# Optimization experiments

Hardware: AMD Instinct MI355X
Metric: run time of the kernel (lower is better)

Reference implementation:

```python
import jax, jax.numpy as jnp
import numpy as np

N_TYPES = 4
N_RELS = 8
N, E, IN_DIM, OUT_DIM = 100000, 1600000, 64, 64
SQRT_DK = float(np.sqrt(OUT_DIM))  # num_heads = 1 -> d_k = out_dim


def setup_inputs() -> dict:
    key = jax.random.key(0)
    ks = jax.random.split(key, 12)
    s = 0.05  # keep activations well-scaled (xavier-ish)
    h = jax.random.normal(ks[0], (N, IN_DIM), jnp.float32)
    node_type = jax.random.randint(ks[1], (N,), 0, N_TYPES, jnp.int32)
    src = jax.random.randint(ks[2], (E,), 0, N, jnp.int32)
    dst = jax.random.randint(ks[3], (E,), 0, N, jnp.int32)
    etype = jax.random.randint(ks[4], (E,), 0, N_RELS, jnp.int32)
    k_lin = jax.random.normal(ks[5], (N_TYPES, IN_DIM, OUT_DIM), jnp.float32) * s
    q_lin = jax.random.normal(ks[6], (N_TYPES, IN_DIM, OUT_DIM), jnp.float32) * s
    v_lin = jax.random.normal(ks[7], (N_TYPES, IN_DIM, OUT_DIM), jnp.float32) * s
    a_lin = jax.random.normal(ks[8], (N_TYPES, OUT_DIM, OUT_DIM), jnp.float32) * s
    rel_att = jax.random.normal(ks[9], (N_RELS, OUT_DIM, OUT_DIM), jnp.float32) * s
    rel_msg = jax.random.normal(ks[10], (N_RELS, OUT_DIM, OUT_DIM), jnp.float32) * s
    rel_pri = jnp.ones((N_RELS,), jnp.float32)
    skip = jnp.ones((N_TYPES,), jnp.float32)
    return dict(h=h, node_type=node_type, src=src, dst=dst, etype=etype,
                k_lin=k_lin, q_lin=q_lin, v_lin=v_lin, a_lin=a_lin,
                rel_att=rel_att, rel_msg=rel_msg, rel_pri=rel_pri, skip=skip)


def _typed_matmul(x, W, node_type):
    # rgnn_relational_matmul_no_scatter_gather_list: per-node-type GEMM.
    # Small fixed loop over node types (4), masked accumulate.
    out = jnp.zeros((x.shape[0], W.shape[-1]), x.dtype)
    for t in range(W.shape[0]):
        out = out + jnp.where((node_type == t)[:, None], x @ W[t], 0.0)
    return out


def reference(h, node_type, src, dst, etype, k_lin, q_lin, v_lin, a_lin,
              rel_att, rel_msg, rel_pri, skip):
    # per-node-type K/Q/V projections (num_heads==1, d_k==out_dim)
    k = _typed_matmul(h, k_lin, node_type)  # [N, d_k]
    q = _typed_matmul(h, q_lin, node_type)  # [N, d_k]
    v = _typed_matmul(h, v_lin, node_type)  # [N, d_k]

    # q @ relation_att, computed per relation for ALL nodes then gathered per edge
    # (avoids materializing [E, d_k, d_k] relation weights per edge)
    qW = jnp.einsum('nd,rde->rne', q, rel_att)  # [R, N, d_k]
    t_edge = qW[etype, dst]                      # [E, d_k]  (dst-side product)
    # attention score: <q_dst @ W_att_r, k_src>
    score = jnp.sum(t_edge * k[src], axis=-1)    # [E]

    # edge softmax over incoming edges of each dst, scaled by pri/sqrt(d_k)
    logits = score * (rel_pri / SQRT_DK)[etype]
    m = jax.ops.segment_max(logits, dst, num_segments=N)
    ex = jnp.exp(logits - m[dst])
    den = jax.ops.segment_sum(ex, dst, num_segments=N)
    alpha = ex / jnp.where(den[dst] == 0, 1.0, den[dst])  # [E]

    # message: v_src @ W_msg_r, per relation then gathered per edge
    vW = jnp.einsum('nd,rde->rne', v, rel_msg)   # [R, N, d_k]
    msg = vW[etype, src]                          # [E, d_k]

    # softmax-weighted aggregation to dst nodes
    agg = jax.ops.segment_sum(alpha[:, None] * msg, dst, num_segments=N)  # [N, d_k]

    # output per-node-type GEMM with sigmoid(skip)-scaled a_linears
    W_out = jax.nn.sigmoid(skip)[:, None, None] * a_lin
    return _typed_matmul(agg, W_out, node_type)  # [N, out_dim]
```

## Files before the change

### kernel.cpp

```cpp
#include <hip/hip_runtime.h>
#include <math.h>

#define DIM 64
#define NT 4
#define NR 8

typedef __attribute__((ext_vector_type(8))) short bf16x8;
typedef __attribute__((ext_vector_type(8))) unsigned short u16x8;
typedef __attribute__((ext_vector_type(4))) float f32x4;

__device__ __forceinline__ unsigned short f2bf(float f) {
    unsigned u = __float_as_uint(f);
    return (unsigned short)((u + 0x7FFF + ((u >> 16) & 1)) >> 16);
}
__device__ __forceinline__ float bf2f(unsigned short u) {
    return __uint_as_float((unsigned)u << 16);
}
__device__ __forceinline__ bf16x8 ldb16(const unsigned short* p) {
    return *((const bf16x8*)p);
}

__global__ void type_count(const int* __restrict__ ntype, int* __restrict__ tm, int N) {
    int i = blockIdx.x * blockDim.x + threadIdx.x;
    int t = (i < N) ? ntype[i] : -1;
    int lane = threadIdx.x & 63;
    #pragma unroll
    for (int tt = 0; tt < NT; tt++) {
        unsigned long long m = __ballot(t == tt);
        int c = __popcll(m);
        if (c && lane == (__ffsll((long long)m) - 1)) atomicAdd(&tm[tt], c);
    }
}

__global__ void type_scan(int* __restrict__ tm) {
    if (threadIdx.x == 0 && blockIdx.x == 0) {
        int b = 0;
        for (int t = 0; t < NT; t++) { tm[4 + t] = b; b += ((tm[t] + 63) >> 6) << 6; }
        tm[12] = b;
    }
}

__global__ void type_scatter(const int* __restrict__ ntype, int* __restrict__ tm,
                             int* __restrict__ order, int N) {
    int i = blockIdx.x * blockDim.x + threadIdx.x;
    int t = (i < N) ? ntype[i] : -1;
    int lane = threadIdx.x & 63;
    #pragma unroll
    for (int tt = 0; tt < NT; tt++) {
        unsigned long long m = __ballot(t == tt);
        int c = __popcll(m);
        if (!c) continue;
        int ldr = __ffsll((long long)m) - 1;
        int base = 0;
        if (lane == ldr) base = atomicAdd(&tm[8 + tt], c);
        base = __shfl(base, ldr, 64);
        if (t == tt) {
            int rank = __popcll(m & ((1ull << lane) - 1ull));
            order[tm[4 + tt] + base + rank] = i;
        }
    }
}

__global__ void prep_all(const float* __restrict__ A, const float* __restrict__ Mw,
                         const float* __restrict__ kl, const float* __restrict__ ql,
                         const float* __restrict__ vl,
                         unsigned short* __restrict__ At, unsigned short* __restrict__ Mt,
                         unsigned short* __restrict__ Wkt, unsigned short* __restrict__ Wqt,
                         unsigned short* __restrict__ Wvt) {
    int i = blockIdx.x * blockDim.x + threadIdx.x;
    if (i >= 28 * DIM * DIM) return;
    int mat = i >> 12;
    int idx = i & 4095;
    int n = idx >> 6;
    int k = idx & 63;
    int so = k * DIM + n;
    if (mat < 8)       At [((size_t)mat << 12) + idx]        = f2bf(A [((size_t)mat << 12) + so]);
    else if (mat < 16) Mt [((size_t)(mat - 8) << 12) + idx]  = f2bf(Mw[((size_t)(mat - 8) << 12) + so]);
    else if (mat < 20) Wkt[((size_t)(mat - 16) << 12) + idx] = f2bf(kl[((size_t)(mat - 16) << 12) + so]);
    else if (mat < 24) Wqt[((size_t)(mat - 20) << 12) + idx] = f2bf(ql[((size_t)(mat - 20) << 12) + so]);
    else               Wvt[((size_t)(mat - 24) << 12) + idx] = f2bf(vl[((size_t)(mat - 24) << 12) + so]);
}

__global__ void __launch_bounds__(256)
proj_mfma(const float* __restrict__ h, const int* __restrict__ ntype,
          const int* __restrict__ order, const int* __restrict__ tm,
          const unsigned short* __restrict__ Wkt, const unsigned short* __restrict__ Wqt,
          const unsigned short* __restrict__ Wvt,
          unsigned short* __restrict__ kvbf, unsigned short* __restrict__ qbf, int N) {
    __shared__ __align__(16) unsigned short xs[64][72];
    int t  = threadIdx.x;
    int n0 = blockIdx.x * 64;
    if (n0 >= tm[12]) return;
    int first = order[n0];
    if (first < 0) return;
    int ty = ntype[first];

    #pragma unroll
    for (int i = 0; i < 4; i++) {
        int idx = t + 256 * i;
        int row = idx >> 4, c4 = idx & 15;
        int gn = order[n0 + row];
        float4 xv = make_float4(0.f, 0.f, 0.f, 0.f);
        if (gn >= 0) xv = ((const float4*)(h + (size_t)gn * DIM))[c4];
        ushort4 b = make_ushort4(f2bf(xv.x), f2bf(xv.y), f2bf(xv.z), f2bf(xv.w));
        *((ushort4*)&xs[row][c4 * 4]) = b;
    }
    __syncthreads();

    int wave = t >> 6, lane = t & 63;
    int m = lane & 15, quad = lane >> 4;
    bf16x8 xa0 = *((const bf16x8*)&xs[wave * 16 + m][quad * 8]);
    bf16x8 xa1 = *((const bf16x8*)&xs[wave * 16 + m][32 + quad * 8]);

    int g[4];
    #pragma unroll
    for (int reg = 0; reg < 4; reg++) g[reg] = order[n0 + wave * 16 + quad * 4 + reg];

    const unsigned short* Wt[3] = { Wkt + (size_t)ty * 4096,
                                    Wqt + (size_t)ty * 4096,
                                    Wvt + (size_t)ty * 4096 };
    for (int mm = 0; mm < 3; mm++) {
        const unsigned short* W = Wt[mm];
        f32x4 c0 = {0.f,0.f,0.f,0.f}, c1 = c0, c2 = c0, c3 = c0;
        c0 = __builtin_amdgcn_mfma_f32_16x16x32_bf16(xa0, ldb16(W + (( 0 + m) << 6)      + quad * 8), c0, 0, 0, 0);
        c1 = __builtin_amdgcn_mfma_f32_16x16x32_bf16(xa0, ldb16(W + ((16 + m) << 6)      + quad * 8), c1, 0, 0, 0);
        c2 = __builtin_amdgcn_mfma_f32_16x16x32_bf16(xa0, ldb16(W + ((32 + m) << 6)      + quad * 8), c2, 0, 0, 0);
        c3 = __builtin_amdgcn_mfma_f32_16x16x32_bf16(xa0, ldb16(W + ((48 + m) << 6)      + quad * 8), c3, 0, 0, 0);
        c0 = __builtin_amdgcn_mfma_f32_16x16x32_bf16(xa1, ldb16(W + (( 0 + m) << 6) + 32 + quad * 8), c0, 0, 0, 0);
        c1 = __builtin_amdgcn_mfma_f32_16x16x32_bf16(xa1, ldb16(W + ((16 + m) << 6) + 32 + quad * 8), c1, 0, 0, 0);
        c2 = __builtin_amdgcn_mfma_f32_16x16x32_bf16(xa1, ldb16(W + ((32 + m) << 6) + 32 + quad * 8), c2, 0, 0, 0);
        c3 = __builtin_amdgcn_mfma_f32_16x16x32_bf16(xa1, ldb16(W + ((48 + m) << 6) + 32 + quad * 8), c3, 0, 0, 0);

        #pragma unroll
        for (int reg = 0; reg < 4; reg++) {
            if (g[reg] < 0) continue;
            unsigned short* row;
            if (mm == 1)       row = qbf  + ((size_t)g[reg] << 6) + m;
            else if (mm == 0)  row = kvbf + ((size_t)g[reg] << 7) + m;
            else               row = kvbf + ((size_t)g[reg] << 7) + 64 + m;
            row[ 0] = f2bf(c0[reg]);
            row[16] = f2bf(c1[reg]);
            row[32] = f2bf(c2[reg]);
            row[48] = f2bf(c3[reg]);
        }
    }
}

__global__ void hist8(const int* __restrict__ dst, const int* __restrict__ et,
                      int* __restrict__ cnt, int E) {
    int e = blockIdx.x * blockDim.x + threadIdx.x;
    if (e < E) atomicAdd(&cnt[dst[e] * NR + et[e]], 1);
}

__global__ void scan1(const int* __restrict__ cnt, int* __restrict__ off,
                      int* __restrict__ bsum, int M) {
    __shared__ int buf[1024];
    int tid = threadIdx.x;
    int i = blockIdx.x * 1024 + tid;
    int x = (i < M) ? cnt[i] : 0;
    buf[tid] = x;
    __syncthreads();
    for (int s = 1; s < 1024; s <<= 1) {
        int t = (tid >= s) ? buf[tid - s] : 0;
        __syncthreads();
        buf[tid] += t;
        __syncthreads();
    }
    if (i < M) off[i] = buf[tid] - x;
    if (tid == 1023) bsum[blockIdx.x] = buf[1023];
}

__global__ void scan2(int* __restrict__ bsum, int nb) {
    __shared__ int buf[1024];
    __shared__ int carry;
    int tid = threadIdx.x;
    if (tid == 0) carry = 0;
    __syncthreads();
    for (int base = 0; base < nb; base += 1024) {
        int i = base + tid;
        int x = (i < nb) ? bsum[i] : 0;
        buf[tid] = x;
        __syncthreads();
        for (int s = 1; s < 1024; s <<= 1) {
            int t = (tid >= s) ? buf[tid - s] : 0;
            __syncthreads();
            buf[tid] += t;
            __syncthreads();
        }
        if (i < nb) bsum[i] = carry + buf[tid] - x;
        __syncthreads();
        if (tid == 1023) carry += buf[1023];
        __syncthreads();
    }
}

__global__ void scan3(int* __restrict__ off, const int* __restrict__ bsum, int M, int E) {
    int i = blockIdx.x * 1024 + threadIdx.x;
    if (i < M) off[i] += bsum[blockIdx.x];
    if (i == 0) off[M] = E;
}

__global__ void scatter8(const int* __restrict__ src, const int* __restrict__ dst,
                         const int* __restrict__ et, const int* __restrict__ off,
                         int* __restrict__ cnt2, int* __restrict__ se, int E) {
    int e = blockIdx.x * blockDim.x + threadIdx.x;
    if (e >= E) return;
    int key = dst[e] * NR + et[e];
    int p = off[key] + atomicAdd(&cnt2[key], 1);
    se[p] = src[e];
}

__global__ void __launch_bounds__(256)
fused_edge(const unsigned short* __restrict__ qbf,
           const unsigned short* __restrict__ kvbf,
           const unsigned short* __restrict__ At,
           const unsigned short* __restrict__ Mt,
           const int* __restrict__ se, const int* __restrict__ off8,
           const float* __restrict__ rel_pri,
           float* __restrict__ agg, int N) {
    __shared__ __align__(16) unsigned short qwb[4][16][72];
    __shared__ __align__(16) unsigned short pl[4][16][72];
    const int t    = threadIdx.x;
    const int wave = t >> 6;
    const int lane = t & 63;
    const int m    = lane & 15;
    const int quad = lane >> 4;
    const int sg   = lane >> 2;
    const int ll   = lane & 3;
    const int n0   = blockIdx.x * 64 + wave * 16;
    if (n0 >= N) return;

    bf16x8 qa0 = {0,0,0,0,0,0,0,0}, qa1 = {0,0,0,0,0,0,0,0};
    {
        const int gn = n0 + m;
        if (gn < N) {
            const unsigned short* qp = qbf + ((size_t)gn << 6) + quad * 8;
            qa0 = *((const bf16x8*)qp);
            qa1 = *((const bf16x8*)(qp + 32));
        }
    }

    const int ob = n0 * NR;
    const int ov0 = off8[ob + lane];
    const int ov1 = off8[ob + 64 + lane];
    const int ov2 = off8[ob + 128];
    const bool act = (n0 + sg) < N;

    f32x4 u0 = {0.f,0.f,0.f,0.f}, u1 = u0, u2 = u0, u3 = u0;
    float ddsum = 0.f;

    for (int r = 0; r < NR; r++) {
        const unsigned short* Ar = At + ((size_t)r << 12);
        f32x4 c0 = {0.f,0.f,0.f,0.f}, c1 = c0, c2 = c0, c3 = c0;
        c0 = __builtin_amdgcn_mfma_f32_16x16x32_bf16(qa0, ldb16(Ar + (( 0 + m) << 6)      + quad * 8), c0, 0, 0, 0);
        c1 = __builtin_amdgcn_mfma_f32_16x16x32_bf16(qa0, ldb16(Ar + ((16 + m) << 6)      + quad * 8), c1, 0, 0, 0);
        c2 = __builtin_amdgcn_mfma_f32_16x16x32_bf16(qa0, ldb16(Ar + ((32 + m) << 6)      + quad * 8), c2, 0, 0, 0);
        c3 = __builtin_amdgcn_mfma_f32_16x16x32_bf16(qa0, ldb16(Ar + ((48 + m) << 6)      + quad * 8), c3, 0, 0, 0);
        c0 = __builtin_amdgcn_mfma_f32_16x16x32_bf16(qa1, ldb16(Ar + (( 0 + m) << 6) + 32 + quad * 8), c0, 0, 0, 0);
        c1 = __builtin_amdgcn_mfma_f32_16x16x32_bf16(qa1, ldb16(Ar + ((16 + m) << 6) + 32 + quad * 8), c1, 0, 0, 0);
        c2 = __builtin_amdgcn_mfma_f32_16x16x32_bf16(qa1, ldb16(Ar + ((32 + m) << 6) + 32 + quad * 8), c2, 0, 0, 0);
        c3 = __builtin_amdgcn_mfma_f32_16x16x32_bf16(qa1, ldb16(Ar + ((48 + m) << 6) + 32 + quad * 8), c3, 0, 0, 0);

        #pragma unroll
        for (int reg = 0; reg < 4; reg++) {
            unsigned short* qr = &qwb[wave][quad * 4 + reg][m];
            qr[ 0] = f2bf(c0[reg]); qr[16] = f2bf(c1[reg]);
            qr[32] = f2bf(c2[reg]); qr[48] = f2bf(c3[reg]);
        }
        asm volatile("s_waitcnt lgkmcnt(0)" ::: "memory");

        const int g  = sg * NR + r;
        const int g1 = g + 1;
        const int x0a = __shfl(ov0, g, 64);
        const int x0b = __shfl(ov1, g - 64, 64);
        int i0 = (g < 64) ? x0a : x0b;
        const int x1a = __shfl(ov0, g1, 64);
        const int x1b = __shfl(ov1, g1 - 64, 64);
        int i1 = (g1 < 64) ? x1a : ((g1 < 128) ? x1b : ov2);
        if (!act) i1 = i0;

        const float pri = rel_pri[r] * 0.125f;
        float pe[16], po[16];
        #pragma unroll
        for (int x = 0; x < 16; x++) { pe[x] = 0.f; po[x] = 0.f; }
        float dde = 0.f, ddo = 0.f;

        if (i0 < i1) {
            const u16x8 tq0 = *((const u16x8*)&qwb[wave][sg][ll * 16]);
            const u16x8 tq1 = *((const u16x8*)&qwb[wave][sg][ll * 16 + 8]);
            float tq[16];
            #pragma unroll
            for (int x = 0; x < 8; x++) { tq[x] = bf2f(tq0[x]); tq[8 + x] = bf2f(tq1[x]); }

            for (int i = i0; i < i1; i += 2) {
                const int sA = se[i];
                const bool hB = (i + 1 < i1);
                const int sB = se[hB ? i + 1 : i];
                const unsigned short* pA = kvbf + ((size_t)sA << 7) + ll * 16;
                const unsigned short* pB = kvbf + ((size_t)sB << 7) + ll * 16;
                const u16x8 kA0 = *((const u16x8*)pA);
                const u16x8 kA1 = *((const u16x8*)(pA + 8));
                const u16x8 vA0 = *((const u16x8*)(pA + 64));
                const u16x8 vA1 = *((const u16x8*)(pA + 72));
                const u16x8 kB0 = *((const u16x8*)pB);
                const u16x8 kB1 = *((const u16x8*)(pB + 8));
                const u16x8 vB0 = *((const u16x8*)(pB + 64));
                const u16x8 vB1 = *((const u16x8*)(pB + 72));
                float sa = 0.f, sb = 0.f;
                #pragma unroll
                for (int x = 0; x < 8; x++) {
                    sa = fmaf(bf2f(kA0[x]), tq[x],     sa);
                    sa = fmaf(bf2f(kA1[x]), tq[8 + x], sa);
                    sb = fmaf(bf2f(kB0[x]), tq[x],     sb);
                    sb = fmaf(bf2f(kB1[x]), tq[8 + x], sb);
                }
                sa += __shfl_xor(sa, 1, 4);
                sa += __shfl_xor(sa, 2, 4);
                sb += __shfl_xor(sb, 1, 4);
                sb += __shfl_xor(sb, 2, 4);
                const float eA = __expf(sa * pri);
                const float eB = hB ? __expf(sb * pri) : 0.f;
                dde += eA; ddo += eB;
                #pragma unroll
                for (int x = 0; x < 8; x++) {
                    pe[x]     = fmaf(eA, bf2f(vA0[x]), pe[x]);
                    pe[8 + x] = fmaf(eA, bf2f(vA1[x]), pe[8 + x]);
                    po[x]     = fmaf(eB, bf2f(vB0[x]), po[x]);
                    po[8 + x] = fmaf(eB, bf2f(vB1[x]), po[8 + x]);
                }
            }
        }
        u16x8 w0, w1;
        #pragma unroll
        for (int x = 0; x < 8; x++) {
            w0[x] = f2bf(pe[x] + po[x]);
            w1[x] = f2bf(pe[8 + x] + po[8 + x]);
        }
        *((u16x8*)&pl[wave][sg][ll * 16])     = w0;
        *((u16x8*)&pl[wave][sg][ll * 16 + 8]) = w1;
        ddsum += dde + ddo;
        asm volatile("s_waitcnt lgkmcnt(0)" ::: "memory");

        const unsigned short* Mr = Mt + ((size_t)r << 12);
        const bf16x8 pa0 = *((const bf16x8*)&pl[wave][m][quad * 8]);
        const bf16x8 pa1 = *((const bf16x8*)&pl[wave][m][32 + quad * 8]);
        u0 = __builtin_amdgcn_mfma_f32_16x16x32_bf16(pa0, ldb16(Mr + (( 0 + m) << 6)      + quad * 8), u0, 0, 0, 0);
        u1 = __builtin_amdgcn_mfma_f32_16x16x32_bf16(pa0, ldb16(Mr + ((16 + m) << 6)      + quad * 8), u1, 0, 0, 0);
        u2 = __builtin_amdgcn_mfma_f32_16x16x32_bf16(pa0, ldb16(Mr + ((32 + m) << 6)      + quad * 8), u2, 0, 0, 0);
        u3 = __builtin_amdgcn_mfma_f32_16x16x32_bf16(pa0, ldb16(Mr + ((48 + m) << 6)      + quad * 8), u3, 0, 0, 0);
        u0 = __builtin_amdgcn_mfma_f32_16x16x32_bf16(pa1, ldb16(Mr + (( 0 + m) << 6) + 32 + quad * 8), u0, 0, 0, 0);
        u1 = __builtin_amdgcn_mfma_f32_16x16x32_bf16(pa1, ldb16(Mr + ((16 + m) << 6) + 32 + quad * 8), u1, 0, 0, 0);
        u2 = __builtin_amdgcn_mfma_f32_16x16x32_bf16(pa1, ldb16(Mr + ((32 + m) << 6) + 32 + quad * 8), u2, 0, 0, 0);
        u3 = __builtin_amdgcn_mfma_f32_16x16x32_bf16(pa1, ldb16(Mr + ((48 + m) << 6) + 32 + quad * 8), u3, 0, 0, 0);
        asm volatile("s_waitcnt lgkmcnt(0)" ::: "memory");
    }

    #pragma unroll
    for (int reg = 0; reg < 4; reg++) {
        const int n = n0 + quad * 4 + reg;
        if (n >= N) continue;
        const float dv  = __shfl(ddsum, (quad * 4 + reg) << 2, 64);
        const float inv = (dv == 0.f) ? 0.f : 1.f / dv;
        float* rowp = agg + ((size_t)n << 6) + m;
        rowp[ 0] = u0[reg] * inv;
        rowp[16] = u1[reg] * inv;
        rowp[32] = u2[reg] * inv;
        rowp[48] = u3[reg] * inv;
    }
}

__global__ void out_typed(const float* __restrict__ agg, const int* __restrict__ ntype,
                          const int* __restrict__ order, const int* __restrict__ tm,
                          const float* __restrict__ Wa, const float* __restrict__ skip,
                          float* __restrict__ out, int N) {
    __shared__ float xs[64][68];
    __shared__ float wsm[64][64];
    int t  = threadIdx.x;
    int n0 = blockIdx.x * 64;
    if (n0 >= tm[12]) return;
    int first = order[n0];
    if (first < 0) return;
    int ty = ntype[first];
    float sg = 1.f / (1.f + expf(-skip[ty]));

    const float4* wg = (const float4*)(Wa + (size_t)ty * DIM * DIM);
    float4* wl = (float4*)&wsm[0][0];
    #pragma unroll
    for (int i = 0; i < 4; i++) {
        float4 w = wg[t + 256 * i];
        w.x *= sg; w.y *= sg; w.z *= sg; w.w *= sg;
        wl[t + 256 * i] = w;
    }
    #pragma unroll
    for (int i = 0; i < 4; i++) {
        int idx = t + 256 * i;
        int row = idx >> 4, c4 = idx & 15;
        int gn = order[n0 + row];
        float4 xv = make_float4(0.f, 0.f, 0.f, 0.f);
        if (gn >= 0) xv = ((const float4*)(agg + (size_t)gn * DIM))[c4];
        ((float4*)&xs[row][0])[c4] = xv;
    }
    __syncthreads();

    int og  = t & 15;
    int ng4 = (t >> 4) * 4;
    float4 a0 = make_float4(0.f,0.f,0.f,0.f), a1 = a0, a2 = a0, a3 = a0;
    #pragma unroll 8
    for (int d = 0; d < DIM; d++) {
        float4 wv = ((const float4*)&wsm[d][0])[og];
        float x0 = xs[ng4 + 0][d];
        float x1 = xs[ng4 + 1][d];
        float x2 = xs[ng4 + 2][d];
        float x3 = xs[ng4 + 3][d];
        a0.x = fmaf(x0, wv.x, a0.x); a0.y = fmaf(x0, wv.y, a0.y);
        a0.z = fmaf(x0, wv.z, a0.z); a0.w = fmaf(x0, wv.w, a0.w);
        a1.x = fmaf(x1, wv.x, a1.x); a1.y = fmaf(x1, wv.y, a1.y);
        a1.z = fmaf(x1, wv.z, a1.z); a1.w = fmaf(x1, wv.w, a1.w);
        a2.x = fmaf(x2, wv.x, a2.x); a2.y = fmaf(x2, wv.y, a2.y);
        a2.z = fmaf(x2, wv.z, a2.z); a2.w = fmaf(x2, wv.w, a2.w);
        a3.x = fmaf(x3, wv.x, a3.x); a3.y = fmaf(x3, wv.y, a3.y);
        a3.z = fmaf(x3, wv.z, a3.z); a3.w = fmaf(x3, wv.w, a3.w);
    }
    int g0 = order[n0 + ng4 + 0];
    int g1 = order[n0 + ng4 + 1];
    int g2 = order[n0 + ng4 + 2];
    int g3 = order[n0 + ng4 + 3];
    if (g0 >= 0) ((float4*)(out + (size_t)g0 * DIM))[og] = a0;
    if (g1 >= 0) ((float4*)(out + (size_t)g1 * DIM))[og] = a1;
    if (g2 >= 0) ((float4*)(out + (size_t)g2 * DIM))[og] = a2;
    if (g3 >= 0) ((float4*)(out + (size_t)g3 * DIM))[og] = a3;
}

extern "C" void kernel_launch(void* const* d_in, const int* in_sizes, int n_in,
                              void* d_out, int out_size, void* d_ws, size_t ws_size,
                              hipStream_t stream) {
    const float* h       = (const float*)d_in[0];
    const int*   ntype   = (const int*)  d_in[1];
    const int*   src     = (const int*)  d_in[2];
    const int*   dst     = (const int*)  d_in[3];
    const int*   et      = (const int*)  d_in[4];
    const float* k_lin   = (const float*)d_in[5];
    const float* q_lin   = (const float*)d_in[6];
    const float* v_lin   = (const float*)d_in[7];
    const float* a_lin   = (const float*)d_in[8];
    const float* rel_att = (const float*)d_in[9];
    const float* rel_msg = (const float*)d_in[10];
    const float* rel_pri = (const float*)d_in[11];
    const float* skip    = (const float*)d_in[12];

    int N = in_sizes[1];
    int E = in_sizes[2];
    int M = N * NR;
    int ocap = N + NT * 64;

    float* ws = (float*)d_ws;
    size_t o = 0;
    unsigned short* kvbf = (unsigned short*)(ws + o); o += (size_t)N * DIM;
    unsigned short* qbf  = (unsigned short*)(ws + o); o += (size_t)N * DIM / 2;
    float* agg  = ws + o; o += (size_t)N * DIM;
    int* off8   = (int*)(ws + o); o += (size_t)M + 1024;
    int* cnt8   = (int*)(ws + o); o += (size_t)M;
    int* cnt28  = (int*)(ws + o); o += (size_t)M;
    int* se     = (int*)(ws + o); o += (size_t)E;
    int* bsum   = (int*)(ws + o); o += 1024;
    int* order  = (int*)(ws + o); o += (size_t)ocap;
    int* tm     = (int*)(ws + o); o += 16;
    unsigned short* At  = (unsigned short*)(ws + o); o += (size_t)NR * DIM * DIM / 2;
    unsigned short* Mt  = (unsigned short*)(ws + o); o += (size_t)NR * DIM * DIM / 2;
    unsigned short* Wkt = (unsigned short*)(ws + o); o += (size_t)NT * DIM * DIM / 2;
    unsigned short* Wqt = (unsigned short*)(ws + o); o += (size_t)NT * DIM * DIM / 2;
    unsigned short* Wvt = (unsigned short*)(ws + o); o += (size_t)NT * DIM * DIM / 2;

    float* out = (float*)d_out;

    hipMemsetAsync(order, 0xFF, (size_t)ocap * 4, stream);
    hipMemsetAsync(tm, 0, 16 * 4, stream);
    hipMemsetAsync(cnt8, 0, (size_t)2 * M * 4, stream);

    type_count<<<(N + 255) / 256, 256, 0, stream>>>(ntype, tm, N);
    type_scan<<<1, 64, 0, stream>>>(tm);
    type_scatter<<<(N + 255) / 256, 256, 0, stream>>>(ntype, tm, order, N);

    prep_all<<<(28 * DIM * DIM + 255) / 256, 256, 0, stream>>>(
        rel_att, rel_msg, k_lin, q_lin, v_lin, At, Mt, Wkt, Wqt, Wvt);

    int gridT = (N + NT * 64 + 63) / 64;
    proj_mfma<<<gridT, 256, 0, stream>>>(h, ntype, order, tm, Wkt, Wqt, Wvt,
                                         kvbf, qbf, N);

    hist8<<<(E + 255) / 256, 256, 0, stream>>>(dst, et, cnt8, E);
    int nb = (M + 1023) / 1024;
    scan1<<<nb, 1024, 0, stream>>>(cnt8, off8, bsum, M);
    scan2<<<1, 1024, 0, stream>>>(bsum, nb);
    scan3<<<nb, 1024, 0, stream>>>(off8, bsum, M, E);
    scatter8<<<(E + 255) / 256, 256, 0, stream>>>(src, dst, et, off8, cnt28, se, E);

    int nb64 = (N + 63) / 64;
    fused_edge<<<nb64, 256, 0, stream>>>(qbf, kvbf, At, Mt, se, off8,
                                         rel_pri, agg, N);

    out_typed<<<gridT, 256, 0, stream>>>(agg, ntype, order, tm, a_lin, skip, out, N);
}
```

Baseline: 654.7 us.

## Process relation pairs per iteration and stage edge source indices in LDS

The fused edge kernel now handles two relations per loop iteration. Each relation gets its own Q·W_att MFMA tile and partial buffer, and the two edge lists are walked in lockstep, so each lane streams edges from two independent relation segments instead of alternating pairs within one. Each wave also preloads up to SE_CAP of its nodes' source indices into shared memory, falling back to global loads beyond that. The aim is more independent gather streams and fewer global index loads, at the cost of more LDS and registers and possible imbalance when the two relation segments differ in length.

```diff
diff --git a/kernel.cpp b/kernel.cpp
--- a/kernel.cpp
+++ b/kernel.cpp
@@ -4,6 +4,7 @@
 #define DIM 64
 #define NT 4
 #define NR 8
+#define SE_CAP 640
 
 typedef __attribute__((ext_vector_type(8))) short bf16x8;
 typedef __attribute__((ext_vector_type(8))) unsigned short u16x8;
@@ -218,8 +219,9 @@
            const int* __restrict__ se, const int* __restrict__ off8,
            const float* __restrict__ rel_pri,
            float* __restrict__ agg, int N) {
-    __shared__ __align__(16) unsigned short qwb[4][16][72];
-    __shared__ __align__(16) unsigned short pl[4][16][72];
+    __shared__ __align__(16) unsigned short qwb[4][2][16][72];
+    __shared__ __align__(16) unsigned short pl[4][2][16][72];
+    __shared__ int sew[4][SE_CAP];
     const int t    = threadIdx.x;
     const int wave = t >> 6;
     const int lane = t & 63;
@@ -240,62 +242,97 @@
         }
     }
 
-    const int ob = n0 * NR;
+    const int ob  = n0 * NR;
     const int ov0 = off8[ob + lane];
     const int ov1 = off8[ob + 64 + lane];
-    const int ov2 = off8[ob + 128];
+    const int eeidx = ((n0 + 16 < N) ? (n0 + 16) : N) * NR;
+    const int ov2 = off8[eeidx];
     const bool act = (n0 + sg) < N;
+
+    const int eb   = __shfl(ov0, 0, 64);
+    const int ecnt = ov2 - eb;
+    const int scnt = (ecnt < SE_CAP) ? ecnt : SE_CAP;
+    for (int i = lane; i < scnt; i += 64) sew[wave][i] = se[eb + i];
 
     f32x4 u0 = {0.f,0.f,0.f,0.f}, u1 = u0, u2 = u0, u3 = u0;
     float ddsum = 0.f;
 
-    for (int r = 0; r < NR; r++) {
-        const unsigned short* Ar = At + ((size_t)r << 12);
+    for (int rp = 0; rp < 4; rp++) {
+        const int r = rp * 2;
+        const unsigned short* Ar  = At + ((size_t)r << 12);
+        const unsigned short* Ar2 = Ar + 4096;
         f32x4 c0 = {0.f,0.f,0.f,0.f}, c1 = c0, c2 = c0, c3 = c0;
-        c0 = __builtin_amdgcn_mfma_f32_16x16x32_bf16(qa0, ldb16(Ar + (( 0 + m) << 6)      + quad * 8), c0, 0, 0, 0);
-        c1 = __builtin_amdgcn_mfma_f32_16x16x32_bf16(qa0, ldb16(Ar + ((16 + m) << 6)      + quad * 8), c1, 0, 0, 0);
-        c2 = __builtin_amdgcn_mfma_f32_16x16x32_bf16(qa0, ldb16(Ar + ((32 + m) << 6)      + quad * 8), c2, 0, 0, 0);
-        c3 = __builtin_amdgcn_mfma_f32_16x16x32_bf16(qa0, ldb16(Ar + ((48 + m) << 6)      + quad * 8), c3, 0, 0, 0);
-        c0 = __builtin_amdgcn_mfma_f32_16x16x32_bf16(qa1, ldb16(Ar + (( 0 + m) << 6) + 32 + quad * 8), c0, 0, 0, 0);
-        c1 = __builtin_amdgcn_mfma_f32_16x16x32_bf16(qa1, ldb16(Ar + ((16 + m) << 6) + 32 + quad * 8), c1, 0, 0, 0);
-        c2 = __builtin_amdgcn_mfma_f32_16x16x32_bf16(qa1, ldb16(Ar + ((32 + m) << 6) + 32 + quad * 8), c2, 0, 0, 0);
-        c3 = __builtin_amdgcn_mfma_f32_16x16x32_bf16(qa1, ldb16(Ar + ((48 + m) << 6) + 32 + quad * 8), c3, 0, 0, 0);
+        f32x4 e0 = c0, e1 = c0, e2 = c0, e3 = c0;
+        c0 = __builtin_amdgcn_mfma_f32_16x16x32_bf16(qa0, ldb16(Ar  + (( 0 + m) << 6)      + quad * 8), c0, 0, 0, 0);
+        c1 = __builtin_amdgcn_mfma_f32_16x16x32_bf16(qa0, ldb16(Ar  + ((16 + m) << 6)      + quad * 8), c1, 0, 0, 0);
+        c2 = __builtin_amdgcn_mfma_f32_16x16x32_bf16(qa0, ldb16(Ar  + ((32 + m) << 6)      + quad * 8), c2, 0, 0, 0);
+        c3 = __builtin_amdgcn_mfma_f32_16x16x32_bf16(qa0, ldb16(Ar  + ((48 + m) << 6)      + quad * 8), c3, 0, 0, 0);
+        c0 = __builtin_amdgcn_mfma_f32_16x16x32_bf16(qa1, ldb16(Ar  + (( 0 + m) << 6) + 32 + quad * 8), c0, 0, 0, 0);
+        c1 = __builtin_amdgcn_mfma_f32_16x16x32_bf16(qa1, ldb16(Ar  + ((16 + m) << 6) + 32 + quad * 8), c1, 0, 0, 0);
+        c2 = __builtin_amdgcn_mfma_f32_16x16x32_bf16(qa1, ldb16(Ar  + ((32 + m) << 6) + 32 + quad * 8), c2, 0, 0, 0);
+        c3 = __builtin_amdgcn_mfma_f32_16x16x32_bf16(qa1, ldb16(Ar  + ((48 + m) << 6) + 32 + quad * 8), c3, 0, 0, 0);
+        e0 = __builtin_amdgcn_mfma_f32_16x16x32_bf16(qa0, ldb16(Ar2 + (( 0 + m) << 6)      + quad * 8), e0, 0, 0, 0);
+        e1 = __builtin_amdgcn_mfma_f32_16x16x32_bf16(qa0, ldb16(Ar2 + ((16 + m) << 6)      + quad * 8), e1, 0, 0, 0);
+        e2 = __builtin_amdgcn_mfma_f32_16x16x32_bf16(qa0, ldb16(Ar2 + ((32 + m) << 6)      + quad * 8), e2, 0, 0, 0);
+        e3 = __builtin_amdgcn_mfma_f32_16x16x32_bf16(qa0, ldb16(Ar2 + ((48 + m) << 6)      + quad * 8), e3, 0, 0, 0);
+        e0 = __builtin_amdgcn_mfma_f32_16x16x32_bf16(qa1, ldb16(Ar2 + (( 0 + m) << 6) + 32 + quad * 8), e0, 0, 0, 0);
+        e1 = __builtin_amdgcn_mfma_f32_16x16x32_bf16(qa1, ldb16(Ar2 + ((16 + m) << 6) + 32 + quad * 8), e1, 0, 0, 0);
+        e2 = __builtin_amdgcn_mfma_f32_16x16x32_bf16(qa1, ldb16(Ar2 + ((32 + m) << 6) + 32 + quad * 8), e2, 0, 0, 0);
+        e3 = __builtin_amdgcn_mfma_f32_16x16x32_bf16(qa1, ldb16(Ar2 + ((48 + m) << 6) + 32 + quad * 8), e3, 0, 0, 0);
 
         #pragma unroll
         for (int reg = 0; reg < 4; reg++) {
-            unsigned short* qr = &qwb[wave][quad * 4 + reg][m];
+            unsigned short* qr = &qwb[wave][0][quad * 4 + reg][m];
             qr[ 0] = f2bf(c0[reg]); qr[16] = f2bf(c1[reg]);
             qr[32] = f2bf(c2[reg]); qr[48] = f2bf(c3[reg]);
+            unsigned short* qr2 = &qwb[wave][1][quad * 4 + reg][m];
+            qr2[ 0] = f2bf(e0[reg]); qr2[16] = f2bf(e1[reg]);
+            qr2[32] = f2bf(e2[reg]); qr2[48] = f2bf(e3[reg]);
         }
         asm volatile("s_waitcnt lgkmcnt(0)" ::: "memory");
 
-        const int g  = sg * NR + r;
-        const int g1 = g + 1;
-        const int x0a = __shfl(ov0, g, 64);
-        const int x0b = __shfl(ov1, g - 64, 64);
-        int i0 = (g < 64) ? x0a : x0b;
-        const int x1a = __shfl(ov0, g1, 64);
-        const int x1b = __shfl(ov1, g1 - 64, 64);
-        int i1 = (g1 < 64) ? x1a : ((g1 < 128) ? x1b : ov2);
-        if (!act) i1 = i0;
-
-        const float pri = rel_pri[r] * 0.125f;
-        float pe[16], po[16];
+        const int gidx = sg * NR + r;
+        const int xa = __shfl(ov0, gidx & 63, 64);
+        const int xb = __shfl(ov1, gidx & 63, 64);
+        const int a0 = (gidx < 64) ? xa : xb;
+        const int g1 = gidx + 1;
+        const int ya = __shfl(ov0, g1 & 63, 64);
+        const int yb = __shfl(ov1, g1 & 63, 64);
+        const int a1 = (g1 < 64) ? ya : ((g1 < 128) ? yb : ov2);
+        const int g2 = gidx + 2;
+        const int za = __shfl(ov0, g2 & 63, 64);
+        const int zb = __shfl(ov1, g2 & 63, 64);
+        const int b1 = (g2 < 64) ? za : ((g2 < 128) ? zb : ov2);
+        const int b0 = a1;
+        int lenA = act ? (a1 - a0) : 0;
+        int lenB = act ? (b1 - b0) : 0;
+        const int nit = (lenA > lenB) ? lenA : lenB;
+
+        float P0[16], P1[16];
         #pragma unroll
-        for (int x = 0; x < 16; x++) { pe[x] = 0.f; po[x] = 0.f; }
-        float dde = 0.f, ddo = 0.f;
-
-        if (i0 < i1) {
-            const u16x8 tq0 = *((const u16x8*)&qwb[wave][sg][ll * 16]);
-            const u16x8 tq1 = *((const u16x8*)&qwb[wave][sg][ll * 16 + 8]);
-            float tq[16];
+        for (int x = 0; x < 16; x++) { P0[x] = 0.f; P1[x] = 0.f; }
+        float dd0 = 0.f, dd1 = 0.f;
+
+        if (nit > 0) {
+            const float priA = rel_pri[r] * 0.125f;
+            const float priB = rel_pri[r + 1] * 0.125f;
+            const u16x8 ta0 = *((const u16x8*)&qwb[wave][0][sg][ll * 16]);
+            const u16x8 ta1 = *((const u16x8*)&qwb[wave][0][sg][ll * 16 + 8]);
+            const u16x8 tb0 = *((const u16x8*)&qwb[wave][1][sg][ll * 16]);
+            const u16x8 tb1 = *((const u16x8*)&qwb[wave][1][sg][ll * 16 + 8]);
+            float tqA[16], tqB[16];
             #pragma unroll
-            for (int x = 0; x < 8; x++) { tq[x] = bf2f(tq0[x]); tq[8 + x] = bf2f(tq1[x]); }
-
-            for (int i = i0; i < i1; i += 2) {
-                const int sA = se[i];
-                const bool hB = (i + 1 < i1);
-                const int sB = se[hB ? i + 1 : i];
+            for (int x = 0; x < 8; x++) {
+                tqA[x] = bf2f(ta0[x]); tqA[8 + x] = bf2f(ta1[x]);
+                tqB[x] = bf2f(tb0[x]); tqB[8 + x] = bf2f(tb1[x]);
+            }
+            for (int it = 0; it < nit; ++it) {
+                const bool vA = it < lenA, vB = it < lenB;
+                const int iA = vA ? a0 + it : eb;
+                const int iB = vB ? b0 + it : eb;
+                const int liA = iA - eb, liB = iB - eb;
+                const int sA = (liA < SE_CAP) ? sew[wave][liA] : se[iA];
+                const int sB = (liB < SE_CAP) ? sew[wave][liB] : se[iB];
                 const unsigned short* pA = kvbf + ((size_t)sA << 7) + ll * 16;
                 const unsigned short* pB = kvbf + ((size_t)sB << 7) + ll * 16;
                 const u16x8 kA0 = *((const u16x8*)pA);
@@ -309,49 +346,62 @@
                 float sa = 0.f, sb = 0.f;
                 #pragma unroll
                 for (int x = 0; x < 8; x++) {
-                    sa = fmaf(bf2f(kA0[x]), tq[x],     sa);
-                    sa = fmaf(bf2f(kA1[x]), tq[8 + x], sa);
-                    sb = fmaf(bf2f(kB0[x]), tq[x],     sb);
-                    sb = fmaf(bf2f(kB1[x]), tq[8 + x], sb);
+                    sa = fmaf(bf2f(kA0[x]), tqA[x],     sa);
+                    sa = fmaf(bf2f(kA1[x]), tqA[8 + x], sa);
+                    sb = fmaf(bf2f(kB0[x]), tqB[x],     sb);
+                    sb = fmaf(bf2f(kB1[x]), tqB[8 + x], sb);
                 }
                 sa += __shfl_xor(sa, 1, 4);
                 sa += __shfl_xor(sa, 2, 4);
                 sb += __shfl_xor(sb, 1, 4);
                 sb += __shfl_xor(sb, 2, 4);
-                const float eA = __expf(sa * pri);
-                const float eB = hB ? __expf(sb * pri) : 0.f;
-                dde += eA; ddo += eB;
+                const float eA = vA ? __expf(sa * priA) : 0.f;
+                const float eB = vB ? __expf(sb * priB) : 0.f;
+                dd0 += eA; dd1 += eB;
                 #pragma unroll
                 for (int x = 0; x < 8; x++) {
-                    pe[x]     = fmaf(eA, bf2f(vA0[x]), pe[x]);
-                    pe[8 + x] = fmaf(eA, bf2f(vA1[x]), pe[8 + x]);
-                    po[x]     = fmaf(eB, bf2f(vB0[x]), po[x]);
-                    po[8 + x] = fmaf(eB, bf2f(vB1[x]), po[8 + x]);
+                    P0[x]     = fmaf(eA, bf2f(vA0[x]), P0[x]);
+                    P0[8 + x] = fmaf(eA, bf2f(vA1[x]), P0[8 + x]);
+                    P1[x]     = fmaf(eB, bf2f(vB0[x]), P1[x]);
+                    P1[8 + x] = fmaf(eB, bf2f(vB1[x]), P1[8 + x]);
                 }
             }
         }
-        u16x8 w0, w1;
+        u16x8 w00, w01, w10, w11;
         #pragma unroll
         for (int x = 0; x < 8; x++) {
-            w0[x] = f2bf(pe[x] + po[x]);
-            w1[x] = f2bf(pe[8 + x] + po[8 + x]);
-        }
-        *((u16x8*)&pl[wave][sg][ll * 16])     = w0;
-        *((u16x8*)&pl[wave][sg][ll * 16 + 8]) = w1;
-        ddsum += dde + ddo;
+            w00[x] = f2bf(P0[x]);     w01[x] = f2bf(P0[8 + x]);
+            w10[x] = f2bf(P1[x]);     w11[x] = f2bf(P1[8 + x]);
+        }
+        *((u16x8*)&pl[wave][0][sg][ll * 16])     = w00;
+        *((u16x8*)&pl[wave][0][sg][ll * 16 + 8]) = w01;
+        *((u16x8*)&pl[wave][1][sg][ll * 16])     = w10;
+        *((u16x8*)&pl[wave][1][sg][ll * 16 + 8]) = w11;
+        ddsum += dd0 + dd1;
         asm volatile("s_waitcnt lgkmcnt(0)" ::: "memory");
 
-        const unsigned short* Mr = Mt + ((size_t)r << 12);
-        const bf16x8 pa0 = *((const bf16x8*)&pl[wave][m][quad * 8]);
-        const bf16x8 pa1 = *((const bf16x8*)&pl[wave][m][32 + quad * 8]);
-        u0 = __builtin_amdgcn_mfma_f32_16x16x32_bf16(pa0, ldb16(Mr + (( 0 + m) << 6)      + quad * 8), u0, 0, 0, 0);
-        u1 = __builtin_amdgcn_mfma_f32_16x16x32_bf16(pa0, ldb16(Mr + ((16 + m) << 6)      + quad * 8), u1, 0, 0, 0);
-        u2 = __builtin_amdgcn_mfma_f32_16x16x32_bf16(pa0, ldb16(Mr + ((32 + m) << 6)      + quad * 8), u2, 0, 0, 0);
-        u3 = __builtin_amdgcn_mfma_f32_16x16x32_bf16(pa0, ldb16(Mr + ((48 + m) << 6)      + quad * 8), u3, 0, 0, 0);
-        u0 = __builtin_amdgcn_mfma_f32_16x16x32_bf16(pa1, ldb16(Mr + (( 0 + m) << 6) + 32 + quad * 8), u0, 0, 0, 0);
-        u1 = __builtin_amdgcn_mfma_f32_16x16x32_bf16(pa1, ldb16(Mr + ((16 + m) << 6) + 32 + quad * 8), u1, 0, 0, 0);
-        u2 = __builtin_amdgcn_mfma_f32_16x16x32_bf16(pa1, ldb16(Mr + ((32 + m) << 6) + 32 + quad * 8), u2, 0, 0, 0);
-        u3 = __builtin_amdgcn_mfma_f32_16x16x32_bf16(pa1, ldb16(Mr + ((48 + m) << 6) + 32 + quad * 8), u3, 0, 0, 0);
+        const unsigned short* Mr  = Mt + ((size_t)r << 12);
+        const unsigned short* Mr2 = Mr + 4096;
+        const bf16x8 pa0 = *((const bf16x8*)&pl[wave][0][m][quad * 8]);
+        const bf16x8 pa1 = *((const bf16x8*)&pl[wave][0][m][32 + quad * 8]);
+        const bf16x8 pb0 = *((const bf16x8*)&pl[wave][1][m][quad * 8]);
+        const bf16x8 pb1 = *((const bf16x8*)&pl[wave][1][m][32 + quad * 8]);
+        u0 = __builtin_amdgcn_mfma_f32_16x16x32_bf16(pa0, ldb16(Mr  + (( 0 + m) << 6)      + quad * 8), u0, 0, 0, 0);
+        u1 = __builtin_amdgcn_mfma_f32_16x16x32_bf16(pa0, ldb16(Mr  + ((16 + m) << 6)      + quad * 8), u1, 0, 0, 0);
+        u2 = __builtin_amdgcn_mfma_f32_16x16x32_bf16(pa0, ldb16(Mr  + ((32 + m) << 6)      + quad * 8), u2, 0, 0, 0);
+        u3 = __builtin_amdgcn_mfma_f32_16x16x32_bf16(pa0, ldb16(Mr  + ((48 + m) << 6)      + quad * 8), u3, 0, 0, 0);
+        u0 = __builtin_amdgcn_mfma_f32_16x16x32_bf16(pa1, ldb16(Mr  + (( 0 + m) << 6) + 32 + quad * 8), u0, 0, 0, 0);
+        u1 = __builtin_amdgcn_mfma_f32_16x16x32_bf16(pa1, ldb16(Mr  + ((16 + m) << 6) + 32 + quad * 8), u1, 0, 0, 0);
+        u2 = __builtin_amdgcn_mfma_f32_16x16x32_bf16(pa1, ldb16(Mr  + ((32 + m) << 6) + 32 + quad * 8), u2, 0, 0, 0);
+        u3 = __builtin_amdgcn_mfma_f32_16x16x32_bf16(pa1, ldb16(Mr  + ((48 + m) << 6) + 32 + quad * 8), u3, 0, 0, 0);
+        u0 = __builtin_amdgcn_mfma_f32_16x16x32_bf16(pb0, ldb16(Mr2 + (( 0 + m) << 6)      + quad * 8), u0, 0, 0, 0);
+        u1 = __builtin_amdgcn_mfma_f32_16x16x32_bf16(pb0, ldb16(Mr2 + ((16 + m) << 6)      + quad * 8), u1, 0, 0, 0);
+        u2 = __builtin_amdgcn_mfma_f32_16x16x32_bf16(pb0, ldb16(Mr2 + ((32 + m) << 6)      + quad * 8), u2, 0, 0, 0);
+        u3 = __builtin_amdgcn_mfma_f32_16x16x32_bf16(pb0, ldb16(Mr2 + ((48 + m) << 6)      + quad * 8), u3, 0, 0, 0);
+        u0 = __builtin_amdgcn_mfma_f32_16x16x32_bf16(pb1, ldb16(Mr2 + (( 0 + m) << 6) + 32 + quad * 8), u0, 0, 0, 0);
+        u1 = __builtin_amdgcn_mfma_f32_16x16x32_bf16(pb1, ldb16(Mr2 + ((16 + m) << 6) + 32 + quad * 8), u1, 0, 0, 0);
+        u2 = __builtin_amdgcn_mfma_f32_16x16x32_bf16(pb1, ldb16(Mr2 + ((32 + m) << 6) + 32 + quad * 8), u2, 0, 0, 0);
+        u3 = __builtin_amdgcn_mfma_f32_16x16x32_bf16(pb1, ldb16(Mr2 + ((48 + m) << 6) + 32 + quad * 8), u3, 0, 0, 0);
         asm volatile("s_waitcnt lgkmcnt(0)" ::: "memory");
     }
 
```

Result: slower. 694.0 us (+6.0%).

## Fold memsets into kernels and project K/Q/V in node order with type masking

Applied to the files above, without the earlier changes.

The three hipMemsetAsync calls are removed: cnt8 and tm are now zeroed inside prep_all, and order is filled with -1 inside type_count. The projection kernel no longer relies on the type-sorted order. It processes nodes in their natural order and runs MFMAs for all four types, zeroing the input rows whose type does not match, which costs four times the projection MFMA work. Outputs are staged through shared memory so each row is written with coalesced 16-byte stores. fused_edge also gets a bounds fix on the end-offset read for the last tile.

```diff
diff --git a/kernel.cpp b/kernel.cpp
--- a/kernel.cpp
+++ b/kernel.cpp
@@ -20,8 +20,33 @@
     return *((const bf16x8*)p);
 }
 
-__global__ void type_count(const int* __restrict__ ntype, int* __restrict__ tm, int N) {
+__global__ void prep_all(const float* __restrict__ A, const float* __restrict__ Mw,
+                         const float* __restrict__ kl, const float* __restrict__ ql,
+                         const float* __restrict__ vl,
+                         unsigned short* __restrict__ At, unsigned short* __restrict__ Mt,
+                         unsigned short* __restrict__ Wkt, unsigned short* __restrict__ Wqt,
+                         unsigned short* __restrict__ Wvt,
+                         int* __restrict__ cnt8, int* __restrict__ tm, int M2) {
     int i = blockIdx.x * blockDim.x + threadIdx.x;
+    if (i < M2) cnt8[i] = 0;
+    if (i < 16) tm[i] = 0;
+    if (i >= 28 * DIM * DIM) return;
+    int mat = i >> 12;
+    int idx = i & 4095;
+    int n = idx >> 6;
+    int k = idx & 63;
+    int so = k * DIM + n;
+    if (mat < 8)       At [((size_t)mat << 12) + idx]        = f2bf(A [((size_t)mat << 12) + so]);
+    else if (mat < 16) Mt [((size_t)(mat - 8) << 12) + idx]  = f2bf(Mw[((size_t)(mat - 8) << 12) + so]);
+    else if (mat < 20) Wkt[((size_t)(mat - 16) << 12) + idx] = f2bf(kl[((size_t)(mat - 16) << 12) + so]);
+    else if (mat < 24) Wqt[((size_t)(mat - 20) << 12) + idx] = f2bf(ql[((size_t)(mat - 20) << 12) + so]);
+    else               Wvt[((size_t)(mat - 24) << 12) + idx] = f2bf(vl[((size_t)(mat - 24) << 12) + so]);
+}
+
+__global__ void type_count(const int* __restrict__ ntype, int* __restrict__ tm,
+                           int* __restrict__ order, int N, int ocap) {
+    int i = blockIdx.x * blockDim.x + threadIdx.x;
+    if (i < ocap) order[i] = -1;
     int t = (i < N) ? ntype[i] : -1;
     int lane = threadIdx.x & 63;
     #pragma unroll
@@ -61,87 +86,74 @@
     }
 }
 
-__global__ void prep_all(const float* __restrict__ A, const float* __restrict__ Mw,
-                         const float* __restrict__ kl, const float* __restrict__ ql,
-                         const float* __restrict__ vl,
-                         unsigned short* __restrict__ At, unsigned short* __restrict__ Mt,
-                         unsigned short* __restrict__ Wkt, unsigned short* __restrict__ Wqt,
-                         unsigned short* __restrict__ Wvt) {
-    int i = blockIdx.x * blockDim.x + threadIdx.x;
-    if (i >= 28 * DIM * DIM) return;
-    int mat = i >> 12;
-    int idx = i & 4095;
-    int n = idx >> 6;
-    int k = idx & 63;
-    int so = k * DIM + n;
-    if (mat < 8)       At [((size_t)mat << 12) + idx]        = f2bf(A [((size_t)mat << 12) + so]);
-    else if (mat < 16) Mt [((size_t)(mat - 8) << 12) + idx]  = f2bf(Mw[((size_t)(mat - 8) << 12) + so]);
-    else if (mat < 20) Wkt[((size_t)(mat - 16) << 12) + idx] = f2bf(kl[((size_t)(mat - 16) << 12) + so]);
-    else if (mat < 24) Wqt[((size_t)(mat - 20) << 12) + idx] = f2bf(ql[((size_t)(mat - 20) << 12) + so]);
-    else               Wvt[((size_t)(mat - 24) << 12) + idx] = f2bf(vl[((size_t)(mat - 24) << 12) + so]);
-}
-
 __global__ void __launch_bounds__(256)
-proj_mfma(const float* __restrict__ h, const int* __restrict__ ntype,
-          const int* __restrict__ order, const int* __restrict__ tm,
+proj_mask(const float* __restrict__ h, const int* __restrict__ ntype,
           const unsigned short* __restrict__ Wkt, const unsigned short* __restrict__ Wqt,
           const unsigned short* __restrict__ Wvt,
           unsigned short* __restrict__ kvbf, unsigned short* __restrict__ qbf, int N) {
     __shared__ __align__(16) unsigned short xs[64][72];
-    int t  = threadIdx.x;
-    int n0 = blockIdx.x * 64;
-    if (n0 >= tm[12]) return;
-    int first = order[n0];
-    if (first < 0) return;
-    int ty = ntype[first];
+    __shared__ __align__(16) unsigned short ot[64][72];
+    const int t  = threadIdx.x;
+    const int n0 = blockIdx.x * 64;
 
     #pragma unroll
     for (int i = 0; i < 4; i++) {
         int idx = t + 256 * i;
         int row = idx >> 4, c4 = idx & 15;
-        int gn = order[n0 + row];
+        int gn = n0 + row;
         float4 xv = make_float4(0.f, 0.f, 0.f, 0.f);
-        if (gn >= 0) xv = ((const float4*)(h + (size_t)gn * DIM))[c4];
-        ushort4 b = make_ushort4(f2bf(xv.x), f2bf(xv.y), f2bf(xv.z), f2bf(xv.w));
-        *((ushort4*)&xs[row][c4 * 4]) = b;
+        if (gn < N) xv = ((const float4*)(h + (size_t)gn * DIM))[c4];
+        *((ushort4*)&xs[row][c4 * 4]) =
+            make_ushort4(f2bf(xv.x), f2bf(xv.y), f2bf(xv.z), f2bf(xv.w));
     }
     __syncthreads();
 
-    int wave = t >> 6, lane = t & 63;
-    int m = lane & 15, quad = lane >> 4;
-    bf16x8 xa0 = *((const bf16x8*)&xs[wave * 16 + m][quad * 8]);
-    bf16x8 xa1 = *((const bf16x8*)&xs[wave * 16 + m][32 + quad * 8]);
-
-    int g[4];
-    #pragma unroll
-    for (int reg = 0; reg < 4; reg++) g[reg] = order[n0 + wave * 16 + quad * 4 + reg];
-
-    const unsigned short* Wt[3] = { Wkt + (size_t)ty * 4096,
-                                    Wqt + (size_t)ty * 4096,
-                                    Wvt + (size_t)ty * 4096 };
+    const int wave = t >> 6, lane = t & 63;
+    const int m = lane & 15, quad = lane >> 4;
+    const bf16x8 xa0 = ldb16(&xs[wave * 16 + m][quad * 8]);
+    const bf16x8 xa1 = ldb16(&xs[wave * 16 + m][32 + quad * 8]);
+    const int myrow = n0 + wave * 16 + m;
+    const int tym = (myrow < N) ? ntype[myrow] : -1;
+    const bf16x8 zz = {0, 0, 0, 0, 0, 0, 0, 0};
+
+    const unsigned short* Wb[3] = { Wkt, Wqt, Wvt };
     for (int mm = 0; mm < 3; mm++) {
-        const unsigned short* W = Wt[mm];
         f32x4 c0 = {0.f,0.f,0.f,0.f}, c1 = c0, c2 = c0, c3 = c0;
-        c0 = __builtin_amdgcn_mfma_f32_16x16x32_bf16(xa0, ldb16(W + (( 0 + m) << 6)      + quad * 8), c0, 0, 0, 0);
-        c1 = __builtin_amdgcn_mfma_f32_16x16x32_bf16(xa0, ldb16(W + ((16 + m) << 6)      + quad * 8), c1, 0, 0, 0);
-        c2 = __builtin_amdgcn_mfma_f32_16x16x32_bf16(xa0, ldb16(W + ((32 + m) << 6)      + quad * 8), c2, 0, 0, 0);
-        c3 = __builtin_amdgcn_mfma_f32_16x16x32_bf16(xa0, ldb16(W + ((48 + m) << 6)      + quad * 8), c3, 0, 0, 0);
-        c0 = __builtin_amdgcn_mfma_f32_16x16x32_bf16(xa1, ldb16(W + (( 0 + m) << 6) + 32 + quad * 8), c0, 0, 0, 0);
-        c1 = __builtin_amdgcn_mfma_f32_16x16x32_bf16(xa1, ldb16(W + ((16 + m) << 6) + 32 + quad * 8), c1, 0, 0, 0);
-        c2 = __builtin_amdgcn_mfma_f32_16x16x32_bf16(xa1, ldb16(W + ((32 + m) << 6) + 32 + quad * 8), c2, 0, 0, 0);
-        c3 = __builtin_amdgcn_mfma_f32_16x16x32_bf16(xa1, ldb16(W + ((48 + m) << 6) + 32 + quad * 8), c3, 0, 0, 0);
-
+        #pragma unroll
+        for (int ty = 0; ty < NT; ty++) {
+            const unsigned short* W = Wb[mm] + ((size_t)ty << 12);
+            const bf16x8 a0 = (tym == ty) ? xa0 : zz;
+            const bf16x8 a1 = (tym == ty) ? xa1 : zz;
+            c0 = __builtin_amdgcn_mfma_f32_16x16x32_bf16(a0, ldb16(W + (( 0 + m) << 6)      + quad * 8), c0, 0, 0, 0);
+            c1 = __builtin_amdgcn_mfma_f32_16x16x32_bf16(a0, ldb16(W + ((16 + m) << 6)      + quad * 8), c1, 0, 0, 0);
+            c2 = __builtin_amdgcn_mfma_f32_16x16x32_bf16(a0, ldb16(W + ((32 + m) << 6)      + quad * 8), c2, 0, 0, 0);
+            c3 = __builtin_amdgcn_mfma_f32_16x16x32_bf16(a0, ldb16(W + ((48 + m) << 6)      + quad * 8), c3, 0, 0, 0);
+            c0 = __builtin_amdgcn_mfma_f32_16x16x32_bf16(a1, ldb16(W + (( 0 + m) << 6) + 32 + quad * 8), c0, 0, 0, 0);
+            c1 = __builtin_amdgcn_mfma_f32_16x16x32_bf16(a1, ldb16(W + ((16 + m) << 6) + 32 + quad * 8), c1, 0, 0, 0);
+            c2 = __builtin_amdgcn_mfma_f32_16x16x32_bf16(a1, ldb16(W + ((32 + m) << 6) + 32 + quad * 8), c2, 0, 0, 0);
+            c3 = __builtin_amdgcn_mfma_f32_16x16x32_bf16(a1, ldb16(W + ((48 + m) << 6) + 32 + quad * 8), c3, 0, 0, 0);
+        }
+        __syncthreads();
         #pragma unroll
         for (int reg = 0; reg < 4; reg++) {
-            if (g[reg] < 0) continue;
-            unsigned short* row;
-            if (mm == 1)       row = qbf  + ((size_t)g[reg] << 6) + m;
-            else if (mm == 0)  row = kvbf + ((size_t)g[reg] << 7) + m;
-            else               row = kvbf + ((size_t)g[reg] << 7) + 64 + m;
-            row[ 0] = f2bf(c0[reg]);
-            row[16] = f2bf(c1[reg]);
-            row[32] = f2bf(c2[reg]);
-            row[48] = f2bf(c3[reg]);
+            unsigned short* qr = &ot[wave * 16 + quad * 4 + reg][m];
+            qr[ 0] = f2bf(c0[reg]); qr[16] = f2bf(c1[reg]);
+            qr[32] = f2bf(c2[reg]); qr[48] = f2bf(c3[reg]);
+        }
+        __syncthreads();
+        #pragma unroll
+        for (int i = 0; i < 2; i++) {
+            int idx = t + 256 * i;
+            int row = idx >> 3, c8 = idx & 7;
+            int gn = n0 + row;
+            if (gn < N) {
+                u16x8 v = *((const u16x8*)&ot[row][c8 * 8]);
+                unsigned short* dp;
+                if (mm == 1)      dp = qbf  + ((size_t)gn << 6) + c8 * 8;
+                else if (mm == 0) dp = kvbf + ((size_t)gn << 7) + c8 * 8;
+                else              dp = kvbf + ((size_t)gn << 7) + 64 + c8 * 8;
+                *((u16x8*)dp) = v;
+            }
         }
     }
 }
@@ -243,7 +255,8 @@
     const int ob = n0 * NR;
     const int ov0 = off8[ob + lane];
     const int ov1 = off8[ob + 64 + lane];
-    const int ov2 = off8[ob + 128];
+    const int eeidx = ((n0 + 16 < N) ? (n0 + 16) : N) * NR;
+    const int ov2 = off8[eeidx];
     const bool act = (n0 + sg) < N;
 
     f32x4 u0 = {0.f,0.f,0.f,0.f}, u1 = u0, u2 = u0, u3 = u0;
@@ -473,20 +486,17 @@
 
     float* out = (float*)d_out;
 
-    hipMemsetAsync(order, 0xFF, (size_t)ocap * 4, stream);
-    hipMemsetAsync(tm, 0, 16 * 4, stream);
-    hipMemsetAsync(cnt8, 0, (size_t)2 * M * 4, stream);
-
-    type_count<<<(N + 255) / 256, 256, 0, stream>>>(ntype, tm, N);
+    int M2 = 2 * M;
+    int gprep = (M2 > 28 * DIM * DIM ? M2 : 28 * DIM * DIM);
+    prep_all<<<(gprep + 255) / 256, 256, 0, stream>>>(
+        rel_att, rel_msg, k_lin, q_lin, v_lin, At, Mt, Wkt, Wqt, Wvt, cnt8, tm, M2);
+
+    type_count<<<(ocap + 255) / 256, 256, 0, stream>>>(ntype, tm, order, N, ocap);
     type_scan<<<1, 64, 0, stream>>>(tm);
     type_scatter<<<(N + 255) / 256, 256, 0, stream>>>(ntype, tm, order, N);
 
-    prep_all<<<(28 * DIM * DIM + 255) / 256, 256, 0, stream>>>(
-        rel_att, rel_msg, k_lin, q_lin, v_lin, At, Mt, Wkt, Wqt, Wvt);
-
-    int gridT = (N + NT * 64 + 63) / 64;
-    proj_mfma<<<gridT, 256, 0, stream>>>(h, ntype, order, tm, Wkt, Wqt, Wvt,
-                                         kvbf, qbf, N);
+    int nb64 = (N + 63) / 64;
+    proj_mask<<<nb64, 256, 0, stream>>>(h, ntype, Wkt, Wqt, Wvt, kvbf, qbf, N);
 
     hist8<<<(E + 255) / 256, 256, 0, stream>>>(dst, et, cnt8, E);
     int nb = (M + 1023) / 1024;
@@ -495,9 +505,9 @@
     scan3<<<nb, 1024, 0, stream>>>(off8, bsum, M, E);
     scatter8<<<(E + 255) / 256, 256, 0, stream>>>(src, dst, et, off8, cnt28, se, E);
 
-    int nb64 = (N + 63) / 64;
     fused_edge<<<nb64, 256, 0, stream>>>(qbf, kvbf, At, Mt, se, off8,
                                          rel_pri, agg, N);
 
+    int gridT = (N + NT * 64 + 63) / 64;
     out_typed<<<gridT, 256, 0, stream>>>(agg, ntype, order, tm, a_lin, skip, out, N);
 }
```

After: 702.8 us. +7.3%, slower.
